# Performance work log

Measured on AMD Instinct MI355X. Metric: run time of the kernel, lower is better.

## Reference

```python
import jax, jax.numpy as jnp
import numpy as np

B, N, D_IN, D_OUT, H = 2, 2048, 1024, 1024, 16
HEAD_DIM = D_OUT // H


def setup_inputs() -> dict:
    key = jax.random.key(0)
    ks = jax.random.split(key, 8)
    s = 0.02
    return {
        "x": jax.random.normal(ks[0], (B, N, D_IN), dtype=jnp.float32),
        "Wq": jax.random.normal(ks[1], (D_IN, D_OUT), dtype=jnp.float32) * s,
        "Wk": jax.random.normal(ks[2], (D_IN, D_OUT), dtype=jnp.float32) * s,
        "Wv": jax.random.normal(ks[3], (D_IN, D_OUT), dtype=jnp.float32) * s,
        "Wo": jax.random.normal(ks[4], (D_OUT, D_OUT), dtype=jnp.float32) * s,
        "bo": jnp.zeros((D_OUT,), dtype=jnp.float32),
        "w": jax.random.uniform(ks[5], (H,), dtype=jnp.float32),
        "v": jax.random.uniform(ks[6], (H,), dtype=jnp.float32),
    }


def reference(x, Wq, Wk, Wv, Wo, bo, w, v):
    b, n, _ = x.shape
    h = w.shape[0]
    hd = Wq.shape[1] // h

    # QKV projections -> [b, h, n, hd]
    def proj(W):
        return (x @ W).reshape(b, n, h, hd).transpose(0, 2, 1, 3)

    q, k, val = proj(Wq), proj(Wk), proj(Wv)

    # relative-distance decay R_hat: [h, n, n]
    pos = jnp.arange(n)
    R = jnp.abs(pos[:, None] - pos[None, :]).astype(x.dtype)  # [n, n]
    wv = w[:, None, None]
    vv = v[:, None, None]
    R_hat = (1.0 + jnp.exp(vv)) / (1.0 + jnp.exp(vv - wv * R))  # [h, n, n]

    # ReLU(QK^T) * R_hat, causal mask, scaled softmax
    scores = jax.nn.relu(jnp.einsum("bhqd,bhkd->bhqk", q, k)) * R_hat[None]
    causal = jnp.triu(jnp.ones((n, n), dtype=bool), k=1)
    scores = jnp.where(causal[None, None], -jnp.inf, scores)
    attn = jax.nn.softmax(scores / np.sqrt(hd).astype(x.dtype), axis=-1)

    ctx = jnp.einsum("bhqk,bhkd->bhqd", attn, val)
    ctx = ctx.transpose(0, 2, 1, 3).reshape(b, n, h * hd)
    return ctx @ Wo + bo
```

## Files before the change

### kernel.cpp

```cpp
#include <hip/hip_runtime.h>

typedef unsigned short u16;
typedef unsigned int u32;
typedef __attribute__((ext_vector_type(8))) short bf16x8;
typedef __attribute__((ext_vector_type(4))) float f32x4;

__device__ __forceinline__ u16 f2bf(float f) {
    u32 u = __float_as_uint(f);
    u += 0x7fffu + ((u >> 16) & 1u);
    return (u16)(u >> 16);
}

#define GL2LDS(gp, lp)                                                                 \
    __builtin_amdgcn_global_load_lds((const __attribute__((address_space(1))) u32*)(const void*)(gp), \
                                     (__attribute__((address_space(3))) u32*)(void*)(lp), 16, 0, 0)

__global__ __launch_bounds__(256) void cast_kernel(const float* __restrict__ src,
                                                   u16* __restrict__ dst, int n4) {
    int i = blockIdx.x * 256 + threadIdx.x;
    if (i >= n4) return;
    float4 val = ((const float4*)src)[i];
    uint2 o;
    o.x = ((u32)f2bf(val.y) << 16) | f2bf(val.x);
    o.y = ((u32)f2bf(val.w) << 16) | f2bf(val.z);
    ((uint2*)dst)[i] = o;
}

__global__ __launch_bounds__(256) void transpose4(const float* __restrict__ Wq,
                                                  const float* __restrict__ Wk,
                                                  const float* __restrict__ Wv,
                                                  const float* __restrict__ Wo,
                                                  u16* __restrict__ Wcat,
                                                  u16* __restrict__ Wot) {
    __shared__ float tl[32][33];
    const int zi = blockIdx.z;
    const float* src = (zi == 0) ? Wq : (zi == 1) ? Wk : (zi == 2) ? Wv : Wo;
    u16* dst = (zi < 3) ? (Wcat + zi * 1048576) : Wot;
    const int tx = threadIdx.x & 31, ty = threadIdx.x >> 5;
    const int kt = blockIdx.y * 32, nt = blockIdx.x * 32;
#pragma unroll
    for (int j = 0; j < 4; ++j)
        tl[ty + j * 8][tx] = src[(kt + ty + j * 8) * 1024 + nt + tx];
    __syncthreads();
#pragma unroll
    for (int j = 0; j < 4; ++j)
        dst[(nt + ty + j * 8) * 1024 + kt + tx] = f2bf(tl[tx][ty + j * 8]);
}

__global__ __launch_bounds__(256) void rtab_kernel(const float* __restrict__ wp,
                                                   const float* __restrict__ vp,
                                                   float* __restrict__ tab) {
    const int i = blockIdx.x * 256 + threadIdx.x;
    const int h = i >> 11, d = i & 2047;
    const float vv = vp[h], ww = wp[h];
    tab[i] = (1.f + expf(vv)) / (1.f + expf(vv - ww * (float)d)) * 0.125f;
}

template <int MODE>
__global__ __launch_bounds__(256, 3) void gemm128(const u16* __restrict__ A,
                                                  const u16* __restrict__ Bt,
                                                  float* __restrict__ C,
                                                  const float* __restrict__ bias,
                                                  u16* __restrict__ Cb,
                                                  u16* __restrict__ Vtb,
                                                  int M, int N, int K) {
    __shared__ __align__(16) u16 As[8192];
    __shared__ __align__(16) u16 Bs[8192];
    const int t = threadIdx.x, lane = t & 63, wv = t >> 6;
    const int l15 = lane & 15, quad = lane >> 4;
    const int m0 = blockIdx.y << 7, n0 = blockIdx.x << 7;
    const int wm = (wv & 1) << 6, wn = (wv >> 1) << 6;

    f32x4 acc[4][4];
#pragma unroll
    for (int i = 0; i < 4; ++i)
#pragma unroll
        for (int j = 0; j < 4; ++j) acc[i][j] = (f32x4){0.f, 0.f, 0.f, 0.f};

    const int lrow = lane >> 3, lchunk = lane & 7;
    for (int k0 = 0; k0 < K; k0 += 64) {
#pragma unroll
        for (int c = 0; c < 4; ++c) {
            const int r0 = wv * 32 + c * 8;
            const int row = r0 + lrow;
            const int g = lchunk ^ (row & 7);
            GL2LDS(A + (size_t)(m0 + row) * K + k0 + g * 8, &As[r0 * 64]);
            GL2LDS(Bt + (size_t)(n0 + row) * K + k0 + g * 8, &Bs[r0 * 64]);
        }
        __syncthreads();
#pragma unroll
        for (int ks = 0; ks < 2; ++ks) {
            const int p = ((ks << 2) | quad) ^ (l15 & 7);
            bf16x8 af[4], bfr[4];
#pragma unroll
            for (int i = 0; i < 4; ++i) {
                af[i] = *(const bf16x8*)&As[(wm + i * 16 + l15) * 64 + p * 8];
                bfr[i] = *(const bf16x8*)&Bs[(wn + i * 16 + l15) * 64 + p * 8];
            }
#pragma unroll
            for (int mb = 0; mb < 4; ++mb)
#pragma unroll
                for (int nb = 0; nb < 4; ++nb)
                    acc[mb][nb] = __builtin_amdgcn_mfma_f32_16x16x32_bf16(af[mb], bfr[nb],
                                                                          acc[mb][nb], 0, 0, 0);
        }
        __syncthreads();
    }
    const int rb = m0 + wm + (quad << 2);
    const int cbase = n0 + wn + l15;
#pragma unroll
    for (int mb = 0; mb < 4; ++mb)
#pragma unroll
        for (int nb = 0; nb < 4; ++nb) {
            const int col = cbase + nb * 16;
#pragma unroll
            for (int r = 0; r < 4; ++r) {
                const int row = rb + mb * 16 + r;
                if (MODE == 0) {
                    C[(size_t)row * N + col] = acc[mb][nb][r] + bias[col];
                } else {
                    if (col < 2048)
                        Cb[(size_t)row * 2048 + col] = f2bf(acc[mb][nb][r]);
                    else
                        Vtb[(size_t)(col - 2048) * 4096 + row] = f2bf(acc[mb][nb][r]);
                }
            }
        }
}

__global__ __launch_bounds__(256, 2) void attn_kernel(const u16* __restrict__ qkb,
                                                      const u16* __restrict__ vtb,
                                                      const float* __restrict__ rtab,
                                                      u16* __restrict__ ctxb) {
    __shared__ __align__(16) u16 Kt[2][4096];
    __shared__ __align__(16) u16 Vt2[2][4096];
    __shared__ __align__(16) u16 Ps[64][76];
    __shared__ float rall[2048];
    __shared__ float lred[4][64];

    const int t = threadIdx.x, lane = t & 63, wv = t >> 6;
    const int l15 = lane & 15, quad = lane >> 4;
    const int z = blockIdx.x, bh = blockIdx.y;
    const int b = bh >> 4, h = bh & 15;

    for (int i = t; i < 2048; i += 256) rall[i] = rtab[(h << 11) + i];

    const int lrow = lane >> 3, lchunk = lane & 7;
    const int half0 = (wv & 1) * 32;

    for (int ph = 0; ph < 2; ++ph) {
        const int qt = ph ? (31 - z) : z;
        const int q0 = qt << 6;

        bf16x8 qa[4][2];
#pragma unroll
        for (int mb = 0; mb < 4; ++mb) {
            const u16* qrow = qkb + (size_t)(b * 2048 + q0 + mb * 16 + l15) * 2048 +
                              (h << 6) + quad * 8;
            qa[mb][0] = *(const bf16x8*)(qrow);
            qa[mb][1] = *(const bf16x8*)(qrow + 32);
        }

        f32x4 cacc[4];
#pragma unroll
        for (int i = 0; i < 4; ++i) cacc[i] = (f32x4){0.f, 0.f, 0.f, 0.f};
        float lacc[4][4] = {};

        {
            const int kg0 = 0;
#pragma unroll
            for (int c = 0; c < 4; ++c) {
                const int r0 = half0 + c * 8;
                const int row = r0 + lrow;
                const int g = lchunk ^ (row & 7);
                if (wv < 2)
                    GL2LDS(qkb + (size_t)(b * 2048 + kg0 + row) * 2048 + 1024 + (h << 6) + g * 8,
                           &Kt[0][r0 * 64]);
                else
                    GL2LDS(vtb + (size_t)((h << 6) + row) * 4096 + b * 2048 + kg0 + g * 8,
                           &Vt2[0][r0 * 64]);
            }
        }

        for (int kt = 0; kt <= qt; ++kt) {
            const int bsel = kt & 1;
            __syncthreads();
            if (kt < qt) {
                const int kg0 = (kt + 1) << 6;
#pragma unroll
                for (int c = 0; c < 4; ++c) {
                    const int r0 = half0 + c * 8;
                    const int row = r0 + lrow;
                    const int g = lchunk ^ (row & 7);
                    if (wv < 2)
                        GL2LDS(qkb + (size_t)(b * 2048 + kg0 + row) * 2048 + 1024 + (h << 6) + g * 8,
                               &Kt[bsel ^ 1][r0 * 64]);
                    else
                        GL2LDS(vtb + (size_t)((h << 6) + row) * 4096 + b * 2048 + kg0 + g * 8,
                               &Vt2[bsel ^ 1][r0 * 64]);
                }
            }

            f32x4 sacc[4];
#pragma unroll
            for (int i = 0; i < 4; ++i) sacc[i] = (f32x4){0.f, 0.f, 0.f, 0.f};
#pragma unroll
            for (int ks = 0; ks < 2; ++ks) {
                const int p = ((ks << 2) | quad) ^ (l15 & 7);
                bf16x8 kb = *(const bf16x8*)&Kt[bsel][((wv << 4) + l15) * 64 + p * 8];
#pragma unroll
                for (int mb = 0; mb < 4; ++mb)
                    sacc[mb] = __builtin_amdgcn_mfma_f32_16x16x32_bf16(qa[mb][ks], kb,
                                                                       sacc[mb], 0, 0, 0);
            }

            const int dbase = q0 - ((kt << 6) + (wv << 4) + l15);
#pragma unroll
            for (int mb = 0; mb < 4; ++mb)
#pragma unroll
                for (int r = 0; r < 4; ++r) {
                    const int dist = dbase + mb * 16 + (quad << 2) + r;
                    const int di = dist < 0 ? 0 : dist;
                    float pe = __expf(fmaxf(sacc[mb][r], 0.f) * rall[di]);
                    pe = (dist < 0) ? 0.f : pe;
                    lacc[mb][r] += pe;
                    Ps[mb * 16 + (quad << 2) + r][(wv << 4) + l15] = f2bf(pe);
                }
            __syncthreads();

#pragma unroll
            for (int ks = 0; ks < 2; ++ks) {
                const int p = ((ks << 2) | quad) ^ (l15 & 7);
                bf16x8 vb = *(const bf16x8*)&Vt2[bsel][((wv << 4) + l15) * 64 + p * 8];
#pragma unroll
                for (int mb = 0; mb < 4; ++mb) {
                    bf16x8 pa = *(const bf16x8*)&Ps[mb * 16 + l15][ks * 32 + quad * 8];
                    cacc[mb] = __builtin_amdgcn_mfma_f32_16x16x32_bf16(pa, vb,
                                                                       cacc[mb], 0, 0, 0);
                }
            }
        }

#pragma unroll
        for (int off = 1; off < 16; off <<= 1)
#pragma unroll
            for (int mb = 0; mb < 4; ++mb)
#pragma unroll
                for (int r = 0; r < 4; ++r)
                    lacc[mb][r] += __shfl_xor(lacc[mb][r], off, 16);
        if (l15 == 0) {
#pragma unroll
            for (int mb = 0; mb < 4; ++mb)
#pragma unroll
                for (int r = 0; r < 4; ++r)
                    lred[wv][mb * 16 + (quad << 2) + r] = lacc[mb][r];
        }
        __syncthreads();
#pragma unroll
        for (int mb = 0; mb < 4; ++mb)
#pragma unroll
            for (int r = 0; r < 4; ++r) {
                const int row = mb * 16 + (quad << 2) + r;
                const float lt = (lred[0][row] + lred[1][row]) + (lred[2][row] + lred[3][row]);
                const float o = cacc[mb][r] / lt;
                ctxb[(size_t)(b * 2048 + q0 + row) * 1024 + (h << 6) + (wv << 4) + l15] = f2bf(o);
            }
        if (ph == 0) __syncthreads();
    }
}

extern "C" void kernel_launch(void* const* d_in, const int* in_sizes, int n_in,
                              void* d_out, int out_size, void* d_ws, size_t ws_size,
                              hipStream_t stream) {
    const float* x  = (const float*)d_in[0];
    const float* Wq = (const float*)d_in[1];
    const float* Wk = (const float*)d_in[2];
    const float* Wv = (const float*)d_in[3];
    const float* Wo = (const float*)d_in[4];
    const float* bo = (const float*)d_in[5];
    const float* w  = (const float*)d_in[6];
    const float* v  = (const float*)d_in[7];
    float* out = (float*)d_out;

    char* w8 = (char*)d_ws;
    u16*  xb   = (u16*)(w8);
    u16*  Wcat = (u16*)(w8 + (8u << 20));
    u16*  Wot  = (u16*)(w8 + (14u << 20));
    u16*  qkb  = (u16*)(w8 + (16u << 20));
    u16*  vtb  = (u16*)(w8 + (32u << 20));
    u16*  ctxb = (u16*)(w8 + (40u << 20));
    float* rtab = (float*)(w8 + (48u << 20));

    cast_kernel<<<4096, 256, 0, stream>>>(x, xb, 1048576);
    transpose4<<<dim3(32, 32, 4), 256, 0, stream>>>(Wq, Wk, Wv, Wo, Wcat, Wot);
    rtab_kernel<<<128, 256, 0, stream>>>(w, v, rtab);

    gemm128<1><<<dim3(24, 32), 256, 0, stream>>>(xb, Wcat, nullptr, nullptr, qkb, vtb,
                                                 4096, 3072, 1024);
    attn_kernel<<<dim3(16, 32), 256, 0, stream>>>(qkb, vtb, rtab, ctxb);
    gemm128<0><<<dim3(8, 32), 256, 0, stream>>>(ctxb, Wot, out, bo, nullptr, nullptr,
                                                4096, 1024, 1024);
}
```

Before: 216.5 us.

## Split attention into one q-tile per block, narrow output GEMM tile

After: 226.4 us. 4.6% more time.

```diff
diff --git a/kernel.cpp b/kernel.cpp
--- a/kernel.cpp
+++ b/kernel.cpp
@@ -56,7 +56,7 @@
     tab[i] = (1.f + expf(vv)) / (1.f + expf(vv - ww * (float)d)) * 0.125f;
 }
 
-template <int MODE>
+template <int MODE, int BN>
 __global__ __launch_bounds__(256, 3) void gemm128(const u16* __restrict__ A,
                                                   const u16* __restrict__ Bt,
                                                   float* __restrict__ C,
@@ -64,18 +64,19 @@
                                                   u16* __restrict__ Cb,
                                                   u16* __restrict__ Vtb,
                                                   int M, int N, int K) {
+    constexpr int NBW = BN / 32;
     __shared__ __align__(16) u16 As[8192];
-    __shared__ __align__(16) u16 Bs[8192];
+    __shared__ __align__(16) u16 Bs[BN * 64];
     const int t = threadIdx.x, lane = t & 63, wv = t >> 6;
     const int l15 = lane & 15, quad = lane >> 4;
-    const int m0 = blockIdx.y << 7, n0 = blockIdx.x << 7;
-    const int wm = (wv & 1) << 6, wn = (wv >> 1) << 6;
-
-    f32x4 acc[4][4];
+    const int m0 = blockIdx.y << 7, n0 = blockIdx.x * BN;
+    const int wm = (wv & 1) << 6, wn = (wv >> 1) * (BN / 2);
+
+    f32x4 acc[4][NBW];
 #pragma unroll
     for (int i = 0; i < 4; ++i)
 #pragma unroll
-        for (int j = 0; j < 4; ++j) acc[i][j] = (f32x4){0.f, 0.f, 0.f, 0.f};
+        for (int j = 0; j < NBW; ++j) acc[i][j] = (f32x4){0.f, 0.f, 0.f, 0.f};
 
     const int lrow = lane >> 3, lchunk = lane & 7;
     for (int k0 = 0; k0 < K; k0 += 64) {
@@ -85,22 +86,29 @@
             const int row = r0 + lrow;
             const int g = lchunk ^ (row & 7);
             GL2LDS(A + (size_t)(m0 + row) * K + k0 + g * 8, &As[r0 * 64]);
+        }
+#pragma unroll
+        for (int c = 0; c < BN / 32; ++c) {
+            const int r0 = wv * (BN / 4) + c * 8;
+            const int row = r0 + lrow;
+            const int g = lchunk ^ (row & 7);
             GL2LDS(Bt + (size_t)(n0 + row) * K + k0 + g * 8, &Bs[r0 * 64]);
         }
         __syncthreads();
 #pragma unroll
         for (int ks = 0; ks < 2; ++ks) {
             const int p = ((ks << 2) | quad) ^ (l15 & 7);
-            bf16x8 af[4], bfr[4];
-#pragma unroll
-            for (int i = 0; i < 4; ++i) {
+            bf16x8 af[4], bfr[NBW];
+#pragma unroll
+            for (int i = 0; i < 4; ++i)
                 af[i] = *(const bf16x8*)&As[(wm + i * 16 + l15) * 64 + p * 8];
-                bfr[i] = *(const bf16x8*)&Bs[(wn + i * 16 + l15) * 64 + p * 8];
-            }
+#pragma unroll
+            for (int j = 0; j < NBW; ++j)
+                bfr[j] = *(const bf16x8*)&Bs[(wn + j * 16 + l15) * 64 + p * 8];
 #pragma unroll
             for (int mb = 0; mb < 4; ++mb)
 #pragma unroll
-                for (int nb = 0; nb < 4; ++nb)
+                for (int nb = 0; nb < NBW; ++nb)
                     acc[mb][nb] = __builtin_amdgcn_mfma_f32_16x16x32_bf16(af[mb], bfr[nb],
                                                                           acc[mb][nb], 0, 0, 0);
         }
@@ -111,7 +119,7 @@
 #pragma unroll
     for (int mb = 0; mb < 4; ++mb)
 #pragma unroll
-        for (int nb = 0; nb < 4; ++nb) {
+        for (int nb = 0; nb < NBW; ++nb) {
             const int col = cbase + nb * 16;
 #pragma unroll
             for (int r = 0; r < 4; ++r) {
@@ -128,7 +136,7 @@
         }
 }
 
-__global__ __launch_bounds__(256, 2) void attn_kernel(const u16* __restrict__ qkb,
+__global__ __launch_bounds__(256, 3) void attn_kernel(const u16* __restrict__ qkb,
                                                       const u16* __restrict__ vtb,
                                                       const float* __restrict__ rtab,
                                                       u16* __restrict__ ctxb) {
@@ -140,34 +148,48 @@
 
     const int t = threadIdx.x, lane = t & 63, wv = t >> 6;
     const int l15 = lane & 15, quad = lane >> 4;
-    const int z = blockIdx.x, bh = blockIdx.y;
+    const int qt = 31 - blockIdx.x;
+    const int bh = blockIdx.y;
     const int b = bh >> 4, h = bh & 15;
-
-    for (int i = t; i < 2048; i += 256) rall[i] = rtab[(h << 11) + i];
+    const int q0 = qt << 6;
+
+    for (int i = t; i < q0 + 64; i += 256) rall[i] = rtab[(h << 11) + i];
 
     const int lrow = lane >> 3, lchunk = lane & 7;
     const int half0 = (wv & 1) * 32;
 
-    for (int ph = 0; ph < 2; ++ph) {
-        const int qt = ph ? (31 - z) : z;
-        const int q0 = qt << 6;
-
-        bf16x8 qa[4][2];
-#pragma unroll
-        for (int mb = 0; mb < 4; ++mb) {
-            const u16* qrow = qkb + (size_t)(b * 2048 + q0 + mb * 16 + l15) * 2048 +
-                              (h << 6) + quad * 8;
-            qa[mb][0] = *(const bf16x8*)(qrow);
-            qa[mb][1] = *(const bf16x8*)(qrow + 32);
-        }
-
-        f32x4 cacc[4];
-#pragma unroll
-        for (int i = 0; i < 4; ++i) cacc[i] = (f32x4){0.f, 0.f, 0.f, 0.f};
-        float lacc[4][4] = {};
-
-        {
-            const int kg0 = 0;
+    bf16x8 qa[4][2];
+#pragma unroll
+    for (int mb = 0; mb < 4; ++mb) {
+        const u16* qrow = qkb + (size_t)(b * 2048 + q0 + mb * 16 + l15) * 2048 +
+                          (h << 6) + quad * 8;
+        qa[mb][0] = *(const bf16x8*)(qrow);
+        qa[mb][1] = *(const bf16x8*)(qrow + 32);
+    }
+
+    f32x4 cacc[4];
+#pragma unroll
+    for (int i = 0; i < 4; ++i) cacc[i] = (f32x4){0.f, 0.f, 0.f, 0.f};
+    float lacc[4][4] = {};
+
+#pragma unroll
+    for (int c = 0; c < 4; ++c) {
+        const int r0 = half0 + c * 8;
+        const int row = r0 + lrow;
+        const int g = lchunk ^ (row & 7);
+        if (wv < 2)
+            GL2LDS(qkb + (size_t)(b * 2048 + row) * 2048 + 1024 + (h << 6) + g * 8,
+                   &Kt[0][r0 * 64]);
+        else
+            GL2LDS(vtb + (size_t)((h << 6) + row) * 4096 + b * 2048 + g * 8,
+                   &Vt2[0][r0 * 64]);
+    }
+
+    for (int kt = 0; kt <= qt; ++kt) {
+        const int bsel = kt & 1;
+        __syncthreads();
+        if (kt < qt) {
+            const int kg0 = (kt + 1) << 6;
 #pragma unroll
             for (int c = 0; c < 4; ++c) {
                 const int r0 = half0 + c * 8;
@@ -175,46 +197,39 @@
                 const int g = lchunk ^ (row & 7);
                 if (wv < 2)
                     GL2LDS(qkb + (size_t)(b * 2048 + kg0 + row) * 2048 + 1024 + (h << 6) + g * 8,
-                           &Kt[0][r0 * 64]);
+                           &Kt[bsel ^ 1][r0 * 64]);
                 else
                     GL2LDS(vtb + (size_t)((h << 6) + row) * 4096 + b * 2048 + kg0 + g * 8,
-                           &Vt2[0][r0 * 64]);
+                           &Vt2[bsel ^ 1][r0 * 64]);
             }
         }
 
-        for (int kt = 0; kt <= qt; ++kt) {
-            const int bsel = kt & 1;
-            __syncthreads();
-            if (kt < qt) {
-                const int kg0 = (kt + 1) << 6;
-#pragma unroll
-                for (int c = 0; c < 4; ++c) {
-                    const int r0 = half0 + c * 8;
-                    const int row = r0 + lrow;
-                    const int g = lchunk ^ (row & 7);
-                    if (wv < 2)
-                        GL2LDS(qkb + (size_t)(b * 2048 + kg0 + row) * 2048 + 1024 + (h << 6) + g * 8,
-                               &Kt[bsel ^ 1][r0 * 64]);
-                    else
-                        GL2LDS(vtb + (size_t)((h << 6) + row) * 4096 + b * 2048 + kg0 + g * 8,
-                               &Vt2[bsel ^ 1][r0 * 64]);
+        f32x4 sacc[4];
+#pragma unroll
+        for (int i = 0; i < 4; ++i) sacc[i] = (f32x4){0.f, 0.f, 0.f, 0.f};
+#pragma unroll
+        for (int ks = 0; ks < 2; ++ks) {
+            const int p = ((ks << 2) | quad) ^ (l15 & 7);
+            bf16x8 kb = *(const bf16x8*)&Kt[bsel][((wv << 4) + l15) * 64 + p * 8];
+#pragma unroll
+            for (int mb = 0; mb < 4; ++mb)
+                sacc[mb] = __builtin_amdgcn_mfma_f32_16x16x32_bf16(qa[mb][ks], kb,
+                                                                   sacc[mb], 0, 0, 0);
+        }
+
+        const int dbase = q0 - ((kt << 6) + (wv << 4) + l15);
+        if (kt < qt) {
+#pragma unroll
+            for (int mb = 0; mb < 4; ++mb)
+#pragma unroll
+                for (int r = 0; r < 4; ++r) {
+                    const int dist = dbase + mb * 16 + (quad << 2) + r;
+                    const float pe = __expf(fmaxf(sacc[mb][r], 0.f) * rall[dist]);
+                    lacc[mb][r] += pe;
+                    Ps[mb * 16 + (quad << 2) + r][(wv << 4) + l15] =
+                        (u16)(__float_as_uint(pe) >> 16);
                 }
-            }
-
-            f32x4 sacc[4];
-#pragma unroll
-            for (int i = 0; i < 4; ++i) sacc[i] = (f32x4){0.f, 0.f, 0.f, 0.f};
-#pragma unroll
-            for (int ks = 0; ks < 2; ++ks) {
-                const int p = ((ks << 2) | quad) ^ (l15 & 7);
-                bf16x8 kb = *(const bf16x8*)&Kt[bsel][((wv << 4) + l15) * 64 + p * 8];
-#pragma unroll
-                for (int mb = 0; mb < 4; ++mb)
-                    sacc[mb] = __builtin_amdgcn_mfma_f32_16x16x32_bf16(qa[mb][ks], kb,
-                                                                       sacc[mb], 0, 0, 0);
-            }
-
-            const int dbase = q0 - ((kt << 6) + (wv << 4) + l15);
+        } else {
 #pragma unroll
             for (int mb = 0; mb < 4; ++mb)
 #pragma unroll
@@ -224,49 +239,49 @@
                     float pe = __expf(fmaxf(sacc[mb][r], 0.f) * rall[di]);
                     pe = (dist < 0) ? 0.f : pe;
                     lacc[mb][r] += pe;
-                    Ps[mb * 16 + (quad << 2) + r][(wv << 4) + l15] = f2bf(pe);
+                    Ps[mb * 16 + (quad << 2) + r][(wv << 4) + l15] =
+                        (u16)(__float_as_uint(pe) >> 16);
                 }
-            __syncthreads();
-
-#pragma unroll
-            for (int ks = 0; ks < 2; ++ks) {
-                const int p = ((ks << 2) | quad) ^ (l15 & 7);
-                bf16x8 vb = *(const bf16x8*)&Vt2[bsel][((wv << 4) + l15) * 64 + p * 8];
-#pragma unroll
-                for (int mb = 0; mb < 4; ++mb) {
-                    bf16x8 pa = *(const bf16x8*)&Ps[mb * 16 + l15][ks * 32 + quad * 8];
-                    cacc[mb] = __builtin_amdgcn_mfma_f32_16x16x32_bf16(pa, vb,
-                                                                       cacc[mb], 0, 0, 0);
-                }
+        }
+        __syncthreads();
+
+#pragma unroll
+        for (int ks = 0; ks < 2; ++ks) {
+            const int p = ((ks << 2) | quad) ^ (l15 & 7);
+            bf16x8 vb = *(const bf16x8*)&Vt2[bsel][((wv << 4) + l15) * 64 + p * 8];
+#pragma unroll
+            for (int mb = 0; mb < 4; ++mb) {
+                bf16x8 pa = *(const bf16x8*)&Ps[mb * 16 + l15][ks * 32 + quad * 8];
+                cacc[mb] = __builtin_amdgcn_mfma_f32_16x16x32_bf16(pa, vb,
+                                                                   cacc[mb], 0, 0, 0);
             }
         }
-
-#pragma unroll
-        for (int off = 1; off < 16; off <<= 1)
-#pragma unroll
-            for (int mb = 0; mb < 4; ++mb)
-#pragma unroll
-                for (int r = 0; r < 4; ++r)
-                    lacc[mb][r] += __shfl_xor(lacc[mb][r], off, 16);
-        if (l15 == 0) {
-#pragma unroll
-            for (int mb = 0; mb < 4; ++mb)
-#pragma unroll
-                for (int r = 0; r < 4; ++r)
-                    lred[wv][mb * 16 + (quad << 2) + r] = lacc[mb][r];
-        }
-        __syncthreads();
+    }
+
+#pragma unroll
+    for (int off = 1; off < 16; off <<= 1)
 #pragma unroll
         for (int mb = 0; mb < 4; ++mb)
 #pragma unroll
-            for (int r = 0; r < 4; ++r) {
-                const int row = mb * 16 + (quad << 2) + r;
-                const float lt = (lred[0][row] + lred[1][row]) + (lred[2][row] + lred[3][row]);
-                const float o = cacc[mb][r] / lt;
-                ctxb[(size_t)(b * 2048 + q0 + row) * 1024 + (h << 6) + (wv << 4) + l15] = f2bf(o);
-            }
-        if (ph == 0) __syncthreads();
-    }
+            for (int r = 0; r < 4; ++r)
+                lacc[mb][r] += __shfl_xor(lacc[mb][r], off, 16);
+    if (l15 == 0) {
+#pragma unroll
+        for (int mb = 0; mb < 4; ++mb)
+#pragma unroll
+            for (int r = 0; r < 4; ++r)
+                lred[wv][mb * 16 + (quad << 2) + r] = lacc[mb][r];
+    }
+    __syncthreads();
+#pragma unroll
+    for (int mb = 0; mb < 4; ++mb)
+#pragma unroll
+        for (int r = 0; r < 4; ++r) {
+            const int row = mb * 16 + (quad << 2) + r;
+            const float lt = (lred[0][row] + lred[1][row]) + (lred[2][row] + lred[3][row]);
+            const float o = cacc[mb][r] / lt;
+            ctxb[(size_t)(b * 2048 + q0 + row) * 1024 + (h << 6) + (wv << 4) + l15] = f2bf(o);
+        }
 }
 
 extern "C" void kernel_launch(void* const* d_in, const int* in_sizes, int n_in,
@@ -295,9 +310,9 @@
     transpose4<<<dim3(32, 32, 4), 256, 0, stream>>>(Wq, Wk, Wv, Wo, Wcat, Wot);
     rtab_kernel<<<128, 256, 0, stream>>>(w, v, rtab);
 
-    gemm128<1><<<dim3(24, 32), 256, 0, stream>>>(xb, Wcat, nullptr, nullptr, qkb, vtb,
-                                                 4096, 3072, 1024);
-    attn_kernel<<<dim3(16, 32), 256, 0, stream>>>(qkb, vtb, rtab, ctxb);
-    gemm128<0><<<dim3(8, 32), 256, 0, stream>>>(ctxb, Wot, out, bo, nullptr, nullptr,
-                                                4096, 1024, 1024);
-}
+    gemm128<1, 128><<<dim3(24, 32), 256, 0, stream>>>(xb, Wcat, nullptr, nullptr, qkb, vtb,
+                                                      4096, 3072, 1024);
+    attn_kernel<<<dim3(32, 32), 256, 0, stream>>>(qkb, vtb, rtab, ctxb);
+    gemm128<0, 64><<<dim3(16, 32), 256, 0, stream>>>(ctxb, Wot, out, bo, nullptr, nullptr,
+                                                     4096, 1024, 1024);
+}
```
